# Kernel optimization log

Measured on AMD Instinct MI355X. Metric: run time of the kernel, lower is better.

The kernel has to match this reference:

```python
import jax, jax.numpy as jnp
import numpy as np


def setup_inputs() -> dict:
    key = jax.random.key(0)
    k1, k2, k3 = jax.random.split(key, 3)
    B, C, L = 4, 64, 4096
    proj_query = jax.random.normal(k1, (B, C, L), dtype=jnp.float32)
    proj_key = jax.random.normal(k2, (B, C, L), dtype=jnp.float32)
    proj_val = jax.random.normal(k3, (B, C, L), dtype=jnp.float32)
    padding_mask = jnp.ones((B, 1, L), dtype=jnp.float32)
    return {
        "proj_query": proj_query,
        "proj_key": proj_key,
        "proj_val": proj_val,
        "padding_mask": padding_mask,
    }


def reference(proj_query, proj_key, proj_val, padding_mask):
    # proj_query/key/val: [B, C, L]; padding_mask: [B, 1, L]
    B, C, L1 = proj_query.shape
    scale = 1.0 / np.sqrt(C).astype(np.float32)
    # energy[b, lq, lk] = sum_c q[b,c,lq] * k[b,c,lk]
    energy = jnp.einsum("bcq,bck->bqk", proj_query, proj_key)
    attention = energy * scale + jnp.log(padding_mask + 1e-6)  # mask broadcasts over lq
    attention = jax.nn.softmax(attention, axis=-1) * padding_mask
    attention_t = jnp.transpose(attention, (0, 2, 1))  # [B, lk, lq]
    # out[b, c, lq] = sum_lk v[b,c,lk] * attention_t[b,lk,lq]
    out = jnp.einsum("bck,bkq->bcq", proj_val, attention_t)
    return out, attention_t
```

## Files before the change

### kernel.cpp

```cpp
#include <hip/hip_runtime.h>
#include <stdint.h>

#define BB 4
#define CCH 64
#define LLEN 4096
#define QS2 0.18033688011112042f
#define TK 64
#define NTB 256
#define TQS 128
#define NTS 512
#define NCHS 4
#define TPS 16
#define TQE 128
#define NTE 512
#define NCHE 4
#define TPE 16

typedef __bf16 bf16;
typedef bf16 bf16x4 __attribute__((ext_vector_type(4)));
typedef bf16 bf16x8 __attribute__((ext_vector_type(8)));
typedef float f32x4 __attribute__((ext_vector_type(4)));

#define EXP2F(x) __builtin_amdgcn_exp2f(x)
#define LOG2F(x) __builtin_amdgcn_logf(x)

__device__ __forceinline__ int swz(int row, int col) {
    return row * 64 + (col ^ ((row & 7) << 3));
}

__device__ __forceinline__ void g2l16(const void* g, void* l) {
    __builtin_amdgcn_global_load_lds(
        (const __attribute__((address_space(1))) void*)g,
        (__attribute__((address_space(3))) void*)l, 16, 0, 0);
}

#define WAITVM0 asm volatile("s_waitcnt vmcnt(0)" ::: "memory")
#define WAITVM16 asm volatile("s_waitcnt vmcnt(16)" ::: "memory")
#define WAITLGKM0 asm volatile("s_waitcnt lgkmcnt(0)" ::: "memory")
#define BAR() __builtin_amdgcn_s_barrier()
#define PRIO(n) __builtin_amdgcn_s_setprio(n)

__device__ __forceinline__ void stage_rows(const bf16* src, bf16* dst, int w, int l) {
#pragma unroll
    for (int i = 0; i < 2; ++i) {
        int ci = w * 2 + i;
        g2l16(src + ci * 512 + l * 8, dst + ci * 512);
    }
}
__device__ __forceinline__ void stage_tile8(const bf16* src, bf16* dst, int w, int l) {
    g2l16(src + w * 512 + l * 8, dst + w * 512);
}

__global__ __launch_bounds__(NTB) void prep_all(
    const float* __restrict__ qg, const float* __restrict__ kg,
    const float* __restrict__ vg, const float* __restrict__ mg,
    bf16* __restrict__ qT, bf16* __restrict__ kT,
    bf16* __restrict__ vF, float* __restrict__ wS, float* __restrict__ wE)
{
    const int tid = threadIdx.x;
    if (blockIdx.x < 512) {
        __shared__ float t[64][65];
        const int isK = blockIdx.x >> 8;
        const int idx = blockIdx.x & 255;
        const int b = idx >> 6;
        const int lt = idx & 63;
        const float* src = (isK ? kg : qg) + (size_t)b * CCH * LLEN + lt * 64;
        bf16* dst = (isK ? kT : qT) + ((size_t)b * LLEN + lt * 64) * 64;

        int c = tid >> 2, x0 = (tid & 3) * 16;
#pragma unroll
        for (int j = 0; j < 4; ++j) {
            float4 f = *(const float4*)&src[(size_t)c * LLEN + x0 + j * 4];
            t[c][x0 + j * 4 + 0] = f.x;
            t[c][x0 + j * 4 + 1] = f.y;
            t[c][x0 + j * 4 + 2] = f.z;
            t[c][x0 + j * 4 + 3] = f.w;
        }
        __syncthreads();
        int lk = tid >> 2;
        int g0 = (tid & 3) * 2;
#pragma unroll
        for (int gi = 0; gi < 2; ++gi) {
            int gg = g0 + gi;
            bf16x8 v;
#pragma unroll
            for (int j = 0; j < 8; ++j) v[j] = (bf16)t[gg * 8 + j][lk];
            *(bf16x8*)&dst[lk * 64 + ((gg ^ (lk & 7)) * 8)] = v;
        }
    } else if (blockIdx.x < 768) {
        const int row = blockIdx.x - 512;
        const int b = row >> 6;
        const int c = row & 63;
        const int mt = c >> 4, cl = c & 15;
        const size_t base = (size_t)row * LLEN;
        const int x0 = tid * 16;
        const int tile = x0 >> 6;
        float f[16];
#pragma unroll
        for (int j = 0; j < 4; ++j) {
            float4 v4 = *(const float4*)&vg[base + x0 + j * 4];
            f[j * 4 + 0] = v4.x; f[j * 4 + 1] = v4.y;
            f[j * 4 + 2] = v4.z; f[j * 4 + 3] = v4.w;
        }
        bf16* vFb = vF + (size_t)(b * 64 + tile) * 4096;
#pragma unroll
        for (int k2 = 0; k2 < 4; ++k2) {
            int rem = (x0 & 63) + 4 * k2;
            int s = rem >> 5, hl = (rem >> 4) & 1, g = (rem >> 2) & 3;
            bf16x4 hv = {(bf16)f[4 * k2 + 0], (bf16)f[4 * k2 + 1],
                         (bf16)f[4 * k2 + 2], (bf16)f[4 * k2 + 3]};
            *(bf16x4*)&vFb[(size_t)(((s * 4 + mt) * 64 + 16 * g + cl) * 8 + hl * 4)] = hv;
        }
    } else {
        const int b = blockIdx.x - 768;
        int x0 = tid * 16;
#pragma unroll
        for (int j = 0; j < 16; ++j) {
            float m = mg[(size_t)b * LLEN + x0 + j];
            float w = m + 1e-6f;
            wS[(size_t)b * LLEN + x0 + j] = LOG2F(w);
            wE[(size_t)b * LLEN + x0 + j] = LOG2F(w * m);
        }
    }
}

__global__ __launch_bounds__(NTS) void attn_stats(
    const bf16* __restrict__ qT, const bf16* __restrict__ kT,
    const float* __restrict__ wS, float* __restrict__ sums,
    float* __restrict__ outp)
{
    __shared__ __align__(16) bf16 kbuf[2][TK * CCH];
    __shared__ __align__(16) float wbuf[2][TK];
    __shared__ float red[4][TQS];

    const int tid = threadIdx.x;
    const int l = tid & 63;
    const int w = tid >> 6;
    const int sl = w & 3;
    const int h = w >> 2;
    const int g = l >> 4;
    const int cl = l & 15;

    const int idx = blockIdx.x;
    const int chunk = idx & (NCHS - 1);
    const int lqt = (idx >> 2) & 31;
    const int b = idx >> 7;
    const int lq0 = lqt * TQS;
    const size_t bL = (size_t)b * LLEN;
    bf16* kflat = &kbuf[0][0];

    {
        size_t o = ((size_t)idx * NTS + tid) * 4;
        *(float4*)&outp[o] = make_float4(0.f, 0.f, 0.f, 0.f);
    }

    stage_rows(qT + (bL + lq0) * 64, kflat, w, l);
    WAITVM0;
    BAR();
    bf16x8 qf[4][2];
#pragma unroll
    for (int st = 0; st < 4; ++st) {
        int row = h * 64 + st * 16 + cl;
        qf[st][0] = *(const bf16x8*)&kflat[swz(row, 8 * g)];
        qf[st][1] = *(const bf16x8*)&kflat[swz(row, 32 + 8 * g)];
    }
    WAITLGKM0;
    BAR();

    const int lkbase = chunk * (TPS * TK);
    stage_tile8(kT + (bL + lkbase) * 64, kbuf[0], w, l);
    if (w == 0 && l < 16) g2l16(wS + bL + lkbase + l * 4, wbuf[0]);
    WAITVM0;
    BAR();

    float sacc[4] = {0.f, 0.f, 0.f, 0.f};
#pragma unroll
    for (int it = 0; it < TPS; ++it) {
        const int cur = it & 1;

        if (it < TPS - 1) {
            stage_tile8(kT + (bL + lkbase + (it + 1) * 64) * 64, kbuf[cur ^ 1], w, l);
            if (w == 0 && l < 16) g2l16(wS + bL + lkbase + (it + 1) * 64 + l * 4, wbuf[cur ^ 1]);
        }

        bf16x8 kf0 = *(const bf16x8*)&kbuf[cur][swz(16 * sl + cl, 8 * g)];
        bf16x8 kf1 = *(const bf16x8*)&kbuf[cur][swz(16 * sl + cl, 32 + 8 * g)];
        float4 wv = *(const float4*)&wbuf[cur][16 * sl + 4 * g];

        PRIO(1);
#pragma unroll
        for (int st = 0; st < 4; ++st) {
            f32x4 e = (f32x4){0.f, 0.f, 0.f, 0.f};
            e = __builtin_amdgcn_mfma_f32_16x16x32_bf16(kf0, qf[st][0], e, 0, 0, 0);
            e = __builtin_amdgcn_mfma_f32_16x16x32_bf16(kf1, qf[st][1], e, 0, 0, 0);
            sacc[st] += EXP2F(fmaf(e[0], QS2, wv.x));
            sacc[st] += EXP2F(fmaf(e[1], QS2, wv.y));
            sacc[st] += EXP2F(fmaf(e[2], QS2, wv.z));
            sacc[st] += EXP2F(fmaf(e[3], QS2, wv.w));
        }
        PRIO(0);

        if (it < TPS - 1) {
            WAITVM0;
            WAITLGKM0;
            BAR();
        }
    }

#pragma unroll
    for (int st = 0; st < 4; ++st) {
        sacc[st] += __shfl_xor(sacc[st], 16);
        sacc[st] += __shfl_xor(sacc[st], 32);
    }
    if (l < 16) {
#pragma unroll
        for (int st = 0; st < 4; ++st) red[sl][h * 64 + st * 16 + l] = sacc[st];
    }
    __syncthreads();
    if (tid < TQS) {
        float s = (red[0][tid] + red[1][tid]) + (red[2][tid] + red[3][tid]);
        sums[(bL + lq0 + tid) * NCHS + chunk] = s;
    }
}

__global__ __launch_bounds__(NTE, 4) void attn_emit(
    const bf16* __restrict__ qT, const bf16* __restrict__ kT,
    const bf16* __restrict__ vF, const float* __restrict__ wE,
    const float* __restrict__ sums, float* __restrict__ outp,
    float* __restrict__ attnT)
{
    __shared__ __align__(16) bf16 kbuf[2][TK * CCH];
    __shared__ __align__(16) bf16 vbuf[2][TK * CCH];
    __shared__ __align__(16) float wbuf[2][TK];

    const int tid = threadIdx.x;
    const int l = tid & 63;
    const int w = tid >> 6;
    const int strip = w * 16;
    const int g = l >> 4;
    const int cl = l & 15;

    const int idx = blockIdx.x;
    const int chunk = idx & (NCHE - 1);
    const int lqt = (idx >> 2) & 31;
    const int b = idx >> 7;
    const int lq0 = lqt * TQE;
    const size_t bL = (size_t)b * LLEN;
    const size_t obase = (size_t)b * CCH * LLEN;
    bf16* kflat = &kbuf[0][0];

    stage_rows(qT + (bL + lq0) * 64, kflat, w, l);
    float ls2;
    {
        float4 a = *(const float4*)&sums[(bL + lq0 + strip + cl) * NCHS];
        float ssum = (a.x + a.y) + (a.z + a.w);
        ls2 = -LOG2F(ssum);
    }
    WAITVM0;
    BAR();
    bf16x8 qf0 = *(const bf16x8*)&kflat[swz(strip + cl, 8 * g)];
    bf16x8 qf1 = *(const bf16x8*)&kflat[swz(strip + cl, 32 + 8 * g)];
    WAITLGKM0;
    BAR();

    {
        const int lk0 = chunk * (TPE * TK);
        stage_tile8(kT + (bL + lk0) * 64, kbuf[0], w, l);
        stage_tile8(vF + (size_t)(b * 64 + (lk0 >> 6)) * 4096, vbuf[0], w, l);
        if (w == 0 && l < 16) g2l16(wE + bL + lk0 + l * 4, wbuf[0]);
    }
    WAITVM0;
    BAR();

    f32x4 o4[4];
#pragma unroll
    for (int t = 0; t < 4; ++t) o4[t] = (f32x4){0.f, 0.f, 0.f, 0.f};

#pragma unroll
    for (int it = 0; it < TPE; ++it) {
        const int cur = it & 1;
        const int lk0 = chunk * (TPE * TK) + it * 64;

        if (it < TPE - 1) {
            stage_tile8(kT + (bL + lk0 + 64) * 64, kbuf[cur ^ 1], w, l);
            stage_tile8(vF + (size_t)(b * 64 + (lk0 >> 6) + 1) * 4096, vbuf[cur ^ 1], w, l);
            if (w == 0 && l < 16) g2l16(wE + bL + lk0 + 64 + l * 4, wbuf[cur ^ 1]);
        }

        f32x4 e4[4];
#pragma unroll
        for (int t = 0; t < 4; ++t) e4[t] = (f32x4){0.f, 0.f, 0.f, 0.f};
        PRIO(1);
#pragma unroll
        for (int t = 0; t < 4; ++t) {
            bf16x8 kf0 = *(const bf16x8*)&kbuf[cur][swz(16 * t + cl, 8 * g)];
            e4[t] = __builtin_amdgcn_mfma_f32_16x16x32_bf16(kf0, qf0, e4[t], 0, 0, 0);
            bf16x8 kf1 = *(const bf16x8*)&kbuf[cur][swz(16 * t + cl, 32 + 8 * g)];
            e4[t] = __builtin_amdgcn_mfma_f32_16x16x32_bf16(kf1, qf1, e4[t], 0, 0, 0);
        }
        PRIO(0);

        float p[4][4];
#pragma unroll
        for (int t = 0; t < 4; ++t) {
            float4 wv = *(const float4*)&wbuf[cur][16 * t + 4 * g];
            p[t][0] = EXP2F(fmaf(e4[t][0], QS2, ls2 + wv.x));
            p[t][1] = EXP2F(fmaf(e4[t][1], QS2, ls2 + wv.y));
            p[t][2] = EXP2F(fmaf(e4[t][2], QS2, ls2 + wv.z));
            p[t][3] = EXP2F(fmaf(e4[t][3], QS2, ls2 + wv.w));
        }

        bf16x8 pb[2];
#pragma unroll
        for (int s = 0; s < 2; ++s)
#pragma unroll
            for (int j = 0; j < 8; ++j)
                pb[s][j] = (bf16)p[2 * s + (j >> 2)][j & 3];
        PRIO(1);
#pragma unroll
        for (int s = 0; s < 2; ++s) {
            bf16x8 vf4[4];
#pragma unroll
            for (int mt = 0; mt < 4; ++mt)
                vf4[mt] = *(const bf16x8*)&vbuf[cur][((s * 4 + mt) * 64 + l) * 8];
#pragma unroll
            for (int mt = 0; mt < 4; ++mt)
                o4[mt] = __builtin_amdgcn_mfma_f32_16x16x32_bf16(
                    vf4[mt], pb[s], o4[mt], 0, 0, 0);
        }
        PRIO(0);

#pragma unroll
        for (int t = 0; t < 4; ++t)
#pragma unroll
            for (int r = 0; r < 4; ++r) {
                int lkg = lk0 + 16 * t + 4 * g + r;
                attnT[(bL + lkg) * LLEN + lq0 + strip + cl] = p[t][r];
            }

        if (it < TPE - 1) {
            WAITVM16;
            WAITLGKM0;
            BAR();
        }
    }

#pragma unroll
    for (int mt = 0; mt < 4; ++mt)
#pragma unroll
        for (int r = 0; r < 4; ++r) {
            int c = 16 * mt + 4 * g + r;
            atomicAdd(&outp[obase + (size_t)c * LLEN + lq0 + strip + cl], o4[mt][r]);
        }
}

extern "C" void kernel_launch(void* const* d_in, const int* in_sizes, int n_in,
                              void* d_out, int out_size, void* d_ws, size_t ws_size,
                              hipStream_t stream) {
    const float* qg = (const float*)d_in[0];
    const float* kg = (const float*)d_in[1];
    const float* vg = (const float*)d_in[2];
    const float* mg = (const float*)d_in[3];
    float* outp = (float*)d_out;
    float* attnT = outp + (size_t)BB * CCH * LLEN;

    char* ws = (char*)d_ws;
    bf16* qT = (bf16*)ws;
    bf16* kT = (bf16*)(ws + (2u << 20));
    bf16* vF = (bf16*)(ws + (4u << 20));
    float* wS = (float*)(ws + (6u << 20));
    float* wE = (float*)(ws + (6u << 20) + (64u << 10));
    float* sums = (float*)(ws + (6u << 20) + (128u << 10));

    prep_all<<<772, NTB, 0, stream>>>(qg, kg, vg, mg, qT, kT, vF, wS, wE);
    attn_stats<<<BB * (LLEN / TQS) * NCHS, NTS, 0, stream>>>(qT, kT, wS, sums, outp);
    attn_emit<<<BB * (LLEN / TQE) * NCHE, NTE, 0, stream>>>(qT, kT, vF, wE, sums, outp, attnT);
}
```

Measured before the change: 115.4 us.

## Fuse stats and emit kernels with cross-block atomic sum and flag barrier

Merges the row-sum kernel and the emit kernel into one launch. The four chunk blocks for each query tile add their partial exp-sums into a global buffer with atomics, then spin on a per-tile counter before the second pass. The zeroing of the output and the sum and flag buffers moves into the prep kernel. This removes one kernel launch and the sums round trip, but correctness now depends on all four chunk blocks of a tile being resident together, and the spin-wait can stall or deadlock if they are not. Both loops also drop from full unroll to unroll 2.

```diff
diff --git a/kernel.cpp b/kernel.cpp
--- a/kernel.cpp
+++ b/kernel.cpp
@@ -7,10 +7,6 @@
 #define QS2 0.18033688011112042f
 #define TK 64
 #define NTB 256
-#define TQS 128
-#define NTS 512
-#define NCHS 4
-#define TPS 16
 #define TQE 128
 #define NTE 512
 #define NCHE 4
@@ -55,7 +51,8 @@
     const float* __restrict__ qg, const float* __restrict__ kg,
     const float* __restrict__ vg, const float* __restrict__ mg,
     bf16* __restrict__ qT, bf16* __restrict__ kT,
-    bf16* __restrict__ vF, float* __restrict__ wS, float* __restrict__ wE)
+    bf16* __restrict__ vF, float* __restrict__ wS, float* __restrict__ wE,
+    float* __restrict__ gsum, int* __restrict__ flags, float* __restrict__ outp)
 {
     const int tid = threadIdx.x;
     if (blockIdx.x < 512) {
@@ -111,7 +108,7 @@
                          (bf16)f[4 * k2 + 2], (bf16)f[4 * k2 + 3]};
             *(bf16x4*)&vFb[(size_t)(((s * 4 + mt) * 64 + 16 * g + cl) * 8 + hl * 4)] = hv;
         }
-    } else {
+    } else if (blockIdx.x < 772) {
         const int b = blockIdx.x - 768;
         int x0 = tid * 16;
 #pragma unroll
@@ -121,112 +118,25 @@
             wS[(size_t)b * LLEN + x0 + j] = LOG2F(w);
             wE[(size_t)b * LLEN + x0 + j] = LOG2F(w * m);
         }
-    }
-}
-
-__global__ __launch_bounds__(NTS) void attn_stats(
+#pragma unroll
+        for (int j = 0; j < 4; ++j)
+            *(float4*)&gsum[(size_t)b * LLEN + tid * 16 + j * 4] =
+                make_float4(0.f, 0.f, 0.f, 0.f);
+        if (tid < 32) flags[b * 32 + tid] = 0;
+    } else {
+        const int z = blockIdx.x - 772;
+        size_t base = ((size_t)z * NTB + tid) * 16;
+#pragma unroll
+        for (int j = 0; j < 4; ++j)
+            *(float4*)&outp[base + j * 4] = make_float4(0.f, 0.f, 0.f, 0.f);
+    }
+}
+
+__global__ __launch_bounds__(NTE, 4) void attn_fused(
     const bf16* __restrict__ qT, const bf16* __restrict__ kT,
-    const float* __restrict__ wS, float* __restrict__ sums,
-    float* __restrict__ outp)
-{
-    __shared__ __align__(16) bf16 kbuf[2][TK * CCH];
-    __shared__ __align__(16) float wbuf[2][TK];
-    __shared__ float red[4][TQS];
-
-    const int tid = threadIdx.x;
-    const int l = tid & 63;
-    const int w = tid >> 6;
-    const int sl = w & 3;
-    const int h = w >> 2;
-    const int g = l >> 4;
-    const int cl = l & 15;
-
-    const int idx = blockIdx.x;
-    const int chunk = idx & (NCHS - 1);
-    const int lqt = (idx >> 2) & 31;
-    const int b = idx >> 7;
-    const int lq0 = lqt * TQS;
-    const size_t bL = (size_t)b * LLEN;
-    bf16* kflat = &kbuf[0][0];
-
-    {
-        size_t o = ((size_t)idx * NTS + tid) * 4;
-        *(float4*)&outp[o] = make_float4(0.f, 0.f, 0.f, 0.f);
-    }
-
-    stage_rows(qT + (bL + lq0) * 64, kflat, w, l);
-    WAITVM0;
-    BAR();
-    bf16x8 qf[4][2];
-#pragma unroll
-    for (int st = 0; st < 4; ++st) {
-        int row = h * 64 + st * 16 + cl;
-        qf[st][0] = *(const bf16x8*)&kflat[swz(row, 8 * g)];
-        qf[st][1] = *(const bf16x8*)&kflat[swz(row, 32 + 8 * g)];
-    }
-    WAITLGKM0;
-    BAR();
-
-    const int lkbase = chunk * (TPS * TK);
-    stage_tile8(kT + (bL + lkbase) * 64, kbuf[0], w, l);
-    if (w == 0 && l < 16) g2l16(wS + bL + lkbase + l * 4, wbuf[0]);
-    WAITVM0;
-    BAR();
-
-    float sacc[4] = {0.f, 0.f, 0.f, 0.f};
-#pragma unroll
-    for (int it = 0; it < TPS; ++it) {
-        const int cur = it & 1;
-
-        if (it < TPS - 1) {
-            stage_tile8(kT + (bL + lkbase + (it + 1) * 64) * 64, kbuf[cur ^ 1], w, l);
-            if (w == 0 && l < 16) g2l16(wS + bL + lkbase + (it + 1) * 64 + l * 4, wbuf[cur ^ 1]);
-        }
-
-        bf16x8 kf0 = *(const bf16x8*)&kbuf[cur][swz(16 * sl + cl, 8 * g)];
-        bf16x8 kf1 = *(const bf16x8*)&kbuf[cur][swz(16 * sl + cl, 32 + 8 * g)];
-        float4 wv = *(const float4*)&wbuf[cur][16 * sl + 4 * g];
-
-        PRIO(1);
-#pragma unroll
-        for (int st = 0; st < 4; ++st) {
-            f32x4 e = (f32x4){0.f, 0.f, 0.f, 0.f};
-            e = __builtin_amdgcn_mfma_f32_16x16x32_bf16(kf0, qf[st][0], e, 0, 0, 0);
-            e = __builtin_amdgcn_mfma_f32_16x16x32_bf16(kf1, qf[st][1], e, 0, 0, 0);
-            sacc[st] += EXP2F(fmaf(e[0], QS2, wv.x));
-            sacc[st] += EXP2F(fmaf(e[1], QS2, wv.y));
-            sacc[st] += EXP2F(fmaf(e[2], QS2, wv.z));
-            sacc[st] += EXP2F(fmaf(e[3], QS2, wv.w));
-        }
-        PRIO(0);
-
-        if (it < TPS - 1) {
-            WAITVM0;
-            WAITLGKM0;
-            BAR();
-        }
-    }
-
-#pragma unroll
-    for (int st = 0; st < 4; ++st) {
-        sacc[st] += __shfl_xor(sacc[st], 16);
-        sacc[st] += __shfl_xor(sacc[st], 32);
-    }
-    if (l < 16) {
-#pragma unroll
-        for (int st = 0; st < 4; ++st) red[sl][h * 64 + st * 16 + l] = sacc[st];
-    }
-    __syncthreads();
-    if (tid < TQS) {
-        float s = (red[0][tid] + red[1][tid]) + (red[2][tid] + red[3][tid]);
-        sums[(bL + lq0 + tid) * NCHS + chunk] = s;
-    }
-}
-
-__global__ __launch_bounds__(NTE, 4) void attn_emit(
-    const bf16* __restrict__ qT, const bf16* __restrict__ kT,
-    const bf16* __restrict__ vF, const float* __restrict__ wE,
-    const float* __restrict__ sums, float* __restrict__ outp,
+    const bf16* __restrict__ vF, const float* __restrict__ wS,
+    const float* __restrict__ wE, float* __restrict__ gsum,
+    int* __restrict__ flags, float* __restrict__ outp,
     float* __restrict__ attnT)
 {
     __shared__ __align__(16) bf16 kbuf[2][TK * CCH];
@@ -247,28 +157,79 @@
     const int lq0 = lqt * TQE;
     const size_t bL = (size_t)b * LLEN;
     const size_t obase = (size_t)b * CCH * LLEN;
-    bf16* kflat = &kbuf[0][0];
-
-    stage_rows(qT + (bL + lq0) * 64, kflat, w, l);
-    float ls2;
-    {
-        float4 a = *(const float4*)&sums[(bL + lq0 + strip + cl) * NCHS];
-        float ssum = (a.x + a.y) + (a.z + a.w);
-        ls2 = -LOG2F(ssum);
-    }
+    const int lkbase = chunk * (TPE * TK);
+    bf16* vflat = &vbuf[0][0];
+
+    stage_rows(qT + (bL + lq0) * 64, vflat, w, l);
+    stage_tile8(kT + (bL + lkbase) * 64, kbuf[0], w, l);
+    if (w == 0 && l < 16) g2l16(wS + bL + lkbase + l * 4, wbuf[0]);
     WAITVM0;
     BAR();
-    bf16x8 qf0 = *(const bf16x8*)&kflat[swz(strip + cl, 8 * g)];
-    bf16x8 qf1 = *(const bf16x8*)&kflat[swz(strip + cl, 32 + 8 * g)];
+    bf16x8 qf0 = *(const bf16x8*)&vflat[swz(strip + cl, 8 * g)];
+    bf16x8 qf1 = *(const bf16x8*)&vflat[swz(strip + cl, 32 + 8 * g)];
     WAITLGKM0;
     BAR();
 
-    {
-        const int lk0 = chunk * (TPE * TK);
-        stage_tile8(kT + (bL + lk0) * 64, kbuf[0], w, l);
-        stage_tile8(vF + (size_t)(b * 64 + (lk0 >> 6)) * 4096, vbuf[0], w, l);
-        if (w == 0 && l < 16) g2l16(wE + bL + lk0 + l * 4, wbuf[0]);
-    }
+    float sa[4] = {0.f, 0.f, 0.f, 0.f};
+#pragma unroll 2
+    for (int it = 0; it < TPE; ++it) {
+        const int cur = it & 1;
+        if (it < TPE - 1) {
+            stage_tile8(kT + (bL + lkbase + (it + 1) * 64) * 64, kbuf[cur ^ 1], w, l);
+            if (w == 0 && l < 16) g2l16(wS + bL + lkbase + (it + 1) * 64 + l * 4, wbuf[cur ^ 1]);
+        }
+
+        f32x4 e4[4];
+#pragma unroll
+        for (int t = 0; t < 4; ++t) e4[t] = (f32x4){0.f, 0.f, 0.f, 0.f};
+        PRIO(1);
+#pragma unroll
+        for (int t = 0; t < 4; ++t) {
+            bf16x8 kf0 = *(const bf16x8*)&kbuf[cur][swz(16 * t + cl, 8 * g)];
+            e4[t] = __builtin_amdgcn_mfma_f32_16x16x32_bf16(kf0, qf0, e4[t], 0, 0, 0);
+            bf16x8 kf1 = *(const bf16x8*)&kbuf[cur][swz(16 * t + cl, 32 + 8 * g)];
+            e4[t] = __builtin_amdgcn_mfma_f32_16x16x32_bf16(kf1, qf1, e4[t], 0, 0, 0);
+        }
+        PRIO(0);
+#pragma unroll
+        for (int t = 0; t < 4; ++t) {
+            float4 wv = *(const float4*)&wbuf[cur][16 * t + 4 * g];
+            sa[t] += EXP2F(fmaf(e4[t][0], QS2, wv.x));
+            sa[t] += EXP2F(fmaf(e4[t][1], QS2, wv.y));
+            sa[t] += EXP2F(fmaf(e4[t][2], QS2, wv.z));
+            sa[t] += EXP2F(fmaf(e4[t][3], QS2, wv.w));
+        }
+
+        if (it < TPE - 1) {
+            WAITVM0;
+            WAITLGKM0;
+            BAR();
+        }
+    }
+
+    float sacc = (sa[0] + sa[1]) + (sa[2] + sa[3]);
+    sacc += __shfl_xor(sacc, 16);
+    sacc += __shfl_xor(sacc, 32);
+    if (l < 16)
+        atomicAdd(&gsum[bL + lq0 + strip + cl], sacc);
+    __syncthreads();
+
+    if (tid == 0) {
+        __threadfence();
+        atomicAdd(&flags[b * 32 + lqt], 1);
+        while (__hip_atomic_load(&flags[b * 32 + lqt], __ATOMIC_ACQUIRE,
+                                 __HIP_MEMORY_SCOPE_AGENT) < NCHE)
+            __builtin_amdgcn_s_sleep(16);
+    }
+    __syncthreads();
+
+    float ssum = __hip_atomic_load(&gsum[bL + lq0 + strip + cl], __ATOMIC_RELAXED,
+                                   __HIP_MEMORY_SCOPE_AGENT);
+    const float ls2 = -LOG2F(ssum);
+
+    stage_tile8(kT + (bL + lkbase) * 64, kbuf[0], w, l);
+    stage_tile8(vF + (size_t)(b * 64 + (lkbase >> 6)) * 4096, vbuf[0], w, l);
+    if (w == 0 && l < 16) g2l16(wE + bL + lkbase + l * 4, wbuf[0]);
     WAITVM0;
     BAR();
 
@@ -276,10 +237,10 @@
 #pragma unroll
     for (int t = 0; t < 4; ++t) o4[t] = (f32x4){0.f, 0.f, 0.f, 0.f};
 
-#pragma unroll
+#pragma unroll 2
     for (int it = 0; it < TPE; ++it) {
         const int cur = it & 1;
-        const int lk0 = chunk * (TPE * TK) + it * 64;
+        const int lk0 = lkbase + it * 64;
 
         if (it < TPE - 1) {
             stage_tile8(kT + (bL + lk0 + 64) * 64, kbuf[cur ^ 1], w, l);
@@ -370,9 +331,11 @@
     bf16* vF = (bf16*)(ws + (4u << 20));
     float* wS = (float*)(ws + (6u << 20));
     float* wE = (float*)(ws + (6u << 20) + (64u << 10));
-    float* sums = (float*)(ws + (6u << 20) + (128u << 10));
-
-    prep_all<<<772, NTB, 0, stream>>>(qg, kg, vg, mg, qT, kT, vF, wS, wE);
-    attn_stats<<<BB * (LLEN / TQS) * NCHS, NTS, 0, stream>>>(qT, kT, wS, sums, outp);
-    attn_emit<<<BB * (LLEN / TQE) * NCHE, NTE, 0, stream>>>(qT, kT, vF, wE, sums, outp, attnT);
-}
+    float* gsum = (float*)(ws + (6u << 20) + (128u << 10));
+    int* flags = (int*)(ws + (6u << 20) + (192u << 10));
+
+    prep_all<<<1028, NTB, 0, stream>>>(qg, kg, vg, mg, qT, kT, vF, wS, wE,
+                                       gsum, flags, outp);
+    attn_fused<<<BB * (LLEN / TQE) * NCHE, NTE, 0, stream>>>(
+        qT, kT, vF, wS, wE, gsum, flags, outp, attnT);
+}
```

Measured after the change: 100.7 us. 1.15x faster.
